# Kernel optimization log

Measured on AMD Instinct MI355X. Metric: run time of the kernel, lower is better.

The kernel has to match this reference:

```python
import jax, jax.numpy as jnp
import numpy as np

# Pitch / YIN hyperparameters (match init_kwargs)
SR = 8000
HOP = int(round(0.01 * SR))        # 80 samples per hop (hop_time=0.01)
F0_MIN = 60
F0_MAX = 400
THRESH = 0.2
TAU_MIN = SR // F0_MAX             # 20  (smallest lag / highest pitch)
TAU_MAX = SR // F0_MIN             # 133 (largest lag / lowest pitch)
W = TAU_MAX                        # YIN integration window
FRAME_LEN = 2 * TAU_MAX            # need W + TAU_MAX samples per frame


def _yin_f0(x):
    """Batched YIN pitch estimator. x: [B, n_samples] -> f0: [B, n_frames-1].

    Vectorizes the original per-sample Python loop over the whole batch and
    all frames in one pass (difference fn -> CMNDF -> thresholded lag pick).
    """
    B, n = x.shape
    n_frames = 1 + (n - FRAME_LEN) // HOP

    # Frame the signal: [B, F, FRAME_LEN]
    starts = jnp.arange(n_frames) * HOP
    idx = starts[:, None] + jnp.arange(FRAME_LEN)[None, :]
    frames = x[:, idx]

    # Difference function d(tau) = sum_j (x[j] - x[j+tau])^2, tau in [0, TAU_MAX]
    taus = jnp.arange(TAU_MAX + 1)
    sidx = taus[:, None] + jnp.arange(W)[None, :]          # [T+1, W]
    shifted = frames[:, :, sidx]                           # [B, F, T+1, W]
    base = frames[:, :, None, :W]                          # [B, F, 1,  W]
    d = jnp.sum((base - shifted) ** 2, axis=-1)            # [B, F, T+1]

    # Cumulative-mean-normalized difference function (CMNDF)
    eps = jnp.asarray(1e-8, x.dtype)
    cum = jnp.cumsum(d[..., 1:], axis=-1)
    tnum = jnp.arange(1, TAU_MAX + 1, dtype=x.dtype)
    cmndf = d[..., 1:] * tnum / jnp.maximum(cum, eps)      # tau = 1..TAU_MAX
    cmndf = jnp.concatenate([jnp.ones_like(cmndf[..., :1]), cmndf], axis=-1)

    # First lag below threshold (restricted to valid pitch range); else unvoiced
    tau_idx = jnp.arange(TAU_MAX + 1)
    cand = (cmndf < THRESH) & (tau_idx >= TAU_MIN)         # [B, F, T+1]
    voiced = jnp.any(cand, axis=-1)
    tau = jnp.argmax(cand, axis=-1)                        # first True
    f0 = jnp.where(
        voiced,
        jnp.asarray(SR, x.dtype) / jnp.maximum(tau, 1).astype(x.dtype),
        jnp.zeros((), x.dtype),
    )
    # Original forward drops the last frame per sample: f0[0, :-1]
    return f0[:, :-1]


def setup_inputs() -> dict:
    key = jax.random.key(0)
    x = jax.random.normal(key, (8, 80000), dtype=jnp.float32)
    return {"x": x}


def reference(x):
    return _yin_f0(x)
```

## Files before the change

### kernel.cpp

```cpp
#include <hip/hip_runtime.h>


#define NF_OUT 996
#define NSAMP  80000
#define BPB    249
#define TH     0.2f
#define EPS    1e-8f
#define INF_I  0x7FFFFFFF

template<int CTRL>
__device__ __forceinline__ float dpp_add16(float x) {
    int t = __builtin_amdgcn_update_dpp(0, __builtin_bit_cast(int, x), CTRL, 0xF, 0xF, false);
    return x + __builtin_bit_cast(float, t);
}
template<int CTRL>
__device__ __forceinline__ int dpp_min16(int x) {
    int t = __builtin_amdgcn_update_dpp(INF_I, x, CTRL, 0xF, 0xF, false);
    return t < x ? t : x;
}
__device__ __forceinline__ float scan16_add(float v) {
    v = dpp_add16<0x111>(v);
    v = dpp_add16<0x112>(v);
    v = dpp_add16<0x114>(v);
    v = dpp_add16<0x118>(v);
    return v;
}
__device__ __forceinline__ int red16_min(int v) {
    v = dpp_min16<0x111>(v);
    v = dpp_min16<0x112>(v);
    v = dpp_min16<0x114>(v);
    v = dpp_min16<0x118>(v);
    return v;
}

#define MAC8(FR, W0, W1, W2) do { float d_;                                    \
    d_=FR.x-W0.y; a1=fmaf(d_,d_,a1); d_=FR.x-W0.z; a2=fmaf(d_,d_,a2);          \
    d_=FR.x-W0.w; a3=fmaf(d_,d_,a3); d_=FR.x-W1.x; a4=fmaf(d_,d_,a4);          \
    d_=FR.x-W1.y; a5=fmaf(d_,d_,a5); d_=FR.x-W1.z; a6=fmaf(d_,d_,a6);          \
    d_=FR.x-W1.w; a7=fmaf(d_,d_,a7); d_=FR.x-W2.x; a8=fmaf(d_,d_,a8);          \
    d_=FR.y-W0.z; a1=fmaf(d_,d_,a1); d_=FR.y-W0.w; a2=fmaf(d_,d_,a2);          \
    d_=FR.y-W1.x; a3=fmaf(d_,d_,a3); d_=FR.y-W1.y; a4=fmaf(d_,d_,a4);          \
    d_=FR.y-W1.z; a5=fmaf(d_,d_,a5); d_=FR.y-W1.w; a6=fmaf(d_,d_,a6);          \
    d_=FR.y-W2.x; a7=fmaf(d_,d_,a7); d_=FR.y-W2.y; a8=fmaf(d_,d_,a8);          \
    d_=FR.z-W0.w; a1=fmaf(d_,d_,a1); d_=FR.z-W1.x; a2=fmaf(d_,d_,a2);          \
    d_=FR.z-W1.y; a3=fmaf(d_,d_,a3); d_=FR.z-W1.z; a4=fmaf(d_,d_,a4);          \
    d_=FR.z-W1.w; a5=fmaf(d_,d_,a5); d_=FR.z-W2.x; a6=fmaf(d_,d_,a6);          \
    d_=FR.z-W2.y; a7=fmaf(d_,d_,a7); d_=FR.z-W2.z; a8=fmaf(d_,d_,a8);          \
    d_=FR.w-W1.x; a1=fmaf(d_,d_,a1); d_=FR.w-W1.y; a2=fmaf(d_,d_,a2);          \
    d_=FR.w-W1.z; a3=fmaf(d_,d_,a3); d_=FR.w-W1.w; a4=fmaf(d_,d_,a4);          \
    d_=FR.w-W2.x; a5=fmaf(d_,d_,a5); d_=FR.w-W2.y; a6=fmaf(d_,d_,a6);          \
    d_=FR.w-W2.z; a7=fmaf(d_,d_,a7); d_=FR.w-W2.w; a8=fmaf(d_,d_,a8);          \
} while (0)

__global__ __launch_bounds__(64) void yin_kernel(const float* __restrict__ x,
                                                 float* __restrict__ out) {
    const int bx = blockIdx.x;
    const int b  = bx / BPB;
    const int fb = bx - b * BPB;
    const float* __restrict__ xrow = x + (size_t)b * NSAMP + (size_t)fb * 320;

    __shared__ __align__(16) float sch[512];
    const int t = threadIdx.x;
    *(float4*)(sch + 4 * t)       = *(const float4*)(xrow + 4 * t);
    *(float4*)(sch + 4 * t + 256) = *(const float4*)(xrow + 4 * t + 256);
    __syncthreads();

    const int q  = t >> 4;
    const int l4 = t & 15;
    const float* f  = sch + 80 * q;
    const float* gp = f + 8 * l4;

    float4 R0 = *(const float4*)(gp);
    float4 R1 = *(const float4*)(gp + 4);
    float4 R2 = *(const float4*)(gp + 8);
    float4 R3;
    const float4 S0 = R0, S1 = R1;
    float a1=0.f,a2=0.f,a3=0.f,a4=0.f,a5=0.f,a6=0.f,a7=0.f,a8=0.f;

    for (int c = 0; c < 32; c += 4) {
        float4 FR;
        R3 = *(const float4*)(gp + 4*c + 12); FR = *(const float4*)(f + 4*c);      MAC8(FR, R0, R1, R2);
        R0 = *(const float4*)(gp + 4*c + 16); FR = *(const float4*)(f + 4*c + 4);  MAC8(FR, R1, R2, R3);
        R1 = *(const float4*)(gp + 4*c + 20); FR = *(const float4*)(f + 4*c + 8);  MAC8(FR, R2, R3, R0);
        R2 = *(const float4*)(gp + 4*c + 24); FR = *(const float4*)(f + 4*c + 12); MAC8(FR, R3, R0, R1);
    }
    const float4 R35 = *(const float4*)(gp + 140);
    {
        float4 FR = *(const float4*)(f + 128);
        MAC8(FR, R0, R1, R2);
    }
    {
        float frx = f[132];
        float d_;
        d_=frx-R1.y; a1=fmaf(d_,d_,a1); d_=frx-R1.z; a2=fmaf(d_,d_,a2);
        d_=frx-R1.w; a3=fmaf(d_,d_,a3); d_=frx-R2.x; a4=fmaf(d_,d_,a4);
        d_=frx-R2.y; a5=fmaf(d_,d_,a5); d_=frx-R2.z; a6=fmaf(d_,d_,a6);
        d_=frx-R2.w; a7=fmaf(d_,d_,a7); d_=frx-R35.x; a8=fmaf(d_,d_,a8);
    }

    float SA[8]  = {S0.x,S0.y,S0.z,S0.w,S1.x,S1.y,S1.z,S1.w};
    float WA[13] = {R0.x,R0.y,R0.z,R0.w,R1.x,R1.y,R1.z,R1.w,
                    R2.x,R2.y,R2.z,R2.w,R35.x};
    float p[5] = {0.f,0.f,0.f,0.f,0.f};
    #pragma unroll
    for (int k = 0; k < 5; ++k) {
        #pragma unroll
        for (int r = 0; r < 8; ++r) {
            float d_ = SA[r] - WA[1 + k + r];
            p[k] = fmaf(d_, d_, p[k]);
        }
    }
    if (l4 < 5) {
        float fA = f[128 + l4];
        #pragma unroll
        for (int k = 0; k < 5; ++k) {
            float d_ = fA - f[257 + l4 + k];
            p[k] = fmaf(d_, d_, p[k]);
        }
    }
    #pragma unroll
    for (int k = 0; k < 5; ++k) p[k] = scan16_add(p[k]);

    float s1=a1, s2=s1+a2, s3=s2+a3, s4=s3+a4, s5=s4+a5, s6=s5+a6, s7=s6+a7, s8=s7+a8;
    float incl = scan16_add(s8);
    float excl = incl - s8;
    float c1=excl+s1, c2=excl+s2, c3=excl+s3, c4=excl+s4,
          c5=excl+s5, c6=excl+s6, c7=excl+s7, c8=excl+s8;

    int best = INF_I;
    const int tb = 8 * l4;
    if (tb+1 >= 20 && a1*(float)(tb+1) < TH*fmaxf(c1,EPS)) best = tb+1;
    if (best==INF_I && tb+2 >= 20 && a2*(float)(tb+2) < TH*fmaxf(c2,EPS)) best = tb+2;
    if (best==INF_I && tb+3 >= 20 && a3*(float)(tb+3) < TH*fmaxf(c3,EPS)) best = tb+3;
    if (best==INF_I && tb+4 >= 20 && a4*(float)(tb+4) < TH*fmaxf(c4,EPS)) best = tb+4;
    if (best==INF_I && tb+5 >= 20 && a5*(float)(tb+5) < TH*fmaxf(c5,EPS)) best = tb+5;
    if (best==INF_I && tb+6 >= 20 && a6*(float)(tb+6) < TH*fmaxf(c6,EPS)) best = tb+6;
    if (best==INF_I && tb+7 >= 20 && a7*(float)(tb+7) < TH*fmaxf(c7,EPS)) best = tb+7;
    if (best==INF_I && tb+8 >= 20 && a8*(float)(tb+8) < TH*fmaxf(c8,EPS)) best = tb+8;
    best = red16_min(best);

    if (l4 == 15) {
        float cum = c8;
        #pragma unroll
        for (int k = 0; k < 5; ++k) {
            cum += p[k];
            if (p[k] * (float)(129 + k) < TH * fmaxf(cum, EPS))
                best = (best < 129 + k) ? best : (129 + k);
        }
        out[(size_t)b * NF_OUT + fb * 4 + q] =
            (best == INF_I) ? 0.0f : 8000.0f / (float)best;
    }
}

extern "C" void kernel_launch(void* const* d_in, const int* in_sizes, int n_in,
                              void* d_out, int out_size, void* d_ws, size_t ws_size,
                              hipStream_t stream) {
    (void)in_sizes; (void)n_in; (void)d_ws; (void)ws_size; (void)out_size;
    const float* x = (const float*)d_in[0];
    float* out = (float*)d_out;
    yin_kernel<<<dim3(8 * BPB), dim3(64), 0, stream>>>(x, out);
}
```

Baseline: 16.41 us.

## Compute YIN difference via autocorrelation plus energy prefix sums

Expands (x_j - x_{j+tau})^2 into energy terms minus twice the cross-correlation, so the inner loop does one FMA per lag/sample instead of a subtract plus an FMA. The shifted-window energy for each lag comes from the frame energy plus an exclusive scan of squared-sample differences across lanes. This cuts VALU work in the hot loop but adds catastrophic-cancellation risk in float32 for the difference function near zero, which could change threshold decisions.

```diff
diff --git a/kernel.cpp b/kernel.cpp
--- a/kernel.cpp
+++ b/kernel.cpp
@@ -33,23 +33,25 @@
     return v;
 }
 
-#define MAC8(FR, W0, W1, W2) do { float d_;                                    \
-    d_=FR.x-W0.y; a1=fmaf(d_,d_,a1); d_=FR.x-W0.z; a2=fmaf(d_,d_,a2);          \
-    d_=FR.x-W0.w; a3=fmaf(d_,d_,a3); d_=FR.x-W1.x; a4=fmaf(d_,d_,a4);          \
-    d_=FR.x-W1.y; a5=fmaf(d_,d_,a5); d_=FR.x-W1.z; a6=fmaf(d_,d_,a6);          \
-    d_=FR.x-W1.w; a7=fmaf(d_,d_,a7); d_=FR.x-W2.x; a8=fmaf(d_,d_,a8);          \
-    d_=FR.y-W0.z; a1=fmaf(d_,d_,a1); d_=FR.y-W0.w; a2=fmaf(d_,d_,a2);          \
-    d_=FR.y-W1.x; a3=fmaf(d_,d_,a3); d_=FR.y-W1.y; a4=fmaf(d_,d_,a4);          \
-    d_=FR.y-W1.z; a5=fmaf(d_,d_,a5); d_=FR.y-W1.w; a6=fmaf(d_,d_,a6);          \
-    d_=FR.y-W2.x; a7=fmaf(d_,d_,a7); d_=FR.y-W2.y; a8=fmaf(d_,d_,a8);          \
-    d_=FR.z-W0.w; a1=fmaf(d_,d_,a1); d_=FR.z-W1.x; a2=fmaf(d_,d_,a2);          \
-    d_=FR.z-W1.y; a3=fmaf(d_,d_,a3); d_=FR.z-W1.z; a4=fmaf(d_,d_,a4);          \
-    d_=FR.z-W1.w; a5=fmaf(d_,d_,a5); d_=FR.z-W2.x; a6=fmaf(d_,d_,a6);          \
-    d_=FR.z-W2.y; a7=fmaf(d_,d_,a7); d_=FR.z-W2.z; a8=fmaf(d_,d_,a8);          \
-    d_=FR.w-W1.x; a1=fmaf(d_,d_,a1); d_=FR.w-W1.y; a2=fmaf(d_,d_,a2);          \
-    d_=FR.w-W1.z; a3=fmaf(d_,d_,a3); d_=FR.w-W1.w; a4=fmaf(d_,d_,a4);          \
-    d_=FR.w-W2.x; a5=fmaf(d_,d_,a5); d_=FR.w-W2.y; a6=fmaf(d_,d_,a6);          \
-    d_=FR.w-W2.z; a7=fmaf(d_,d_,a7); d_=FR.w-W2.w; a8=fmaf(d_,d_,a8);          \
+#define MACR8(FR, W0, W1, W2) do {                                             \
+    r1=fmaf(FR.x,W0.y,r1); r2=fmaf(FR.x,W0.z,r2);                              \
+    r3=fmaf(FR.x,W0.w,r3); r4=fmaf(FR.x,W1.x,r4);                              \
+    r5=fmaf(FR.x,W1.y,r5); r6=fmaf(FR.x,W1.z,r6);                              \
+    r7=fmaf(FR.x,W1.w,r7); r8=fmaf(FR.x,W2.x,r8);                              \
+    r1=fmaf(FR.y,W0.z,r1); r2=fmaf(FR.y,W0.w,r2);                              \
+    r3=fmaf(FR.y,W1.x,r3); r4=fmaf(FR.y,W1.y,r4);                              \
+    r5=fmaf(FR.y,W1.z,r5); r6=fmaf(FR.y,W1.w,r6);                              \
+    r7=fmaf(FR.y,W2.x,r7); r8=fmaf(FR.y,W2.y,r8);                              \
+    r1=fmaf(FR.z,W0.w,r1); r2=fmaf(FR.z,W1.x,r2);                              \
+    r3=fmaf(FR.z,W1.y,r3); r4=fmaf(FR.z,W1.z,r4);                              \
+    r5=fmaf(FR.z,W1.w,r5); r6=fmaf(FR.z,W2.x,r6);                              \
+    r7=fmaf(FR.z,W2.y,r7); r8=fmaf(FR.z,W2.z,r8);                              \
+    r1=fmaf(FR.w,W1.x,r1); r2=fmaf(FR.w,W1.y,r2);                              \
+    r3=fmaf(FR.w,W1.z,r3); r4=fmaf(FR.w,W1.w,r4);                              \
+    r5=fmaf(FR.w,W2.x,r5); r6=fmaf(FR.w,W2.y,r6);                              \
+    r7=fmaf(FR.w,W2.z,r7); r8=fmaf(FR.w,W2.w,r8);                              \
+    QF=fmaf(FR.x,FR.x,QF); QF=fmaf(FR.y,FR.y,QF);                              \
+    QF=fmaf(FR.z,FR.z,QF); QF=fmaf(FR.w,FR.w,QF);                              \
 } while (0)
 
 __global__ __launch_bounds__(64) void yin_kernel(const float* __restrict__ x,
@@ -75,28 +77,55 @@
     float4 R2 = *(const float4*)(gp + 8);
     float4 R3;
     const float4 S0 = R0, S1 = R1;
-    float a1=0.f,a2=0.f,a3=0.f,a4=0.f,a5=0.f,a6=0.f,a7=0.f,a8=0.f;
+    float r1=0.f,r2=0.f,r3=0.f,r4=0.f,r5=0.f,r6=0.f,r7=0.f,r8=0.f,QF=0.f;
 
     for (int c = 0; c < 32; c += 4) {
         float4 FR;
-        R3 = *(const float4*)(gp + 4*c + 12); FR = *(const float4*)(f + 4*c);      MAC8(FR, R0, R1, R2);
-        R0 = *(const float4*)(gp + 4*c + 16); FR = *(const float4*)(f + 4*c + 4);  MAC8(FR, R1, R2, R3);
-        R1 = *(const float4*)(gp + 4*c + 20); FR = *(const float4*)(f + 4*c + 8);  MAC8(FR, R2, R3, R0);
-        R2 = *(const float4*)(gp + 4*c + 24); FR = *(const float4*)(f + 4*c + 12); MAC8(FR, R3, R0, R1);
+        R3 = *(const float4*)(gp + 4*c + 12); FR = *(const float4*)(f + 4*c);      MACR8(FR, R0, R1, R2);
+        R0 = *(const float4*)(gp + 4*c + 16); FR = *(const float4*)(f + 4*c + 4);  MACR8(FR, R1, R2, R3);
+        R1 = *(const float4*)(gp + 4*c + 20); FR = *(const float4*)(f + 4*c + 8);  MACR8(FR, R2, R3, R0);
+        R2 = *(const float4*)(gp + 4*c + 24); FR = *(const float4*)(f + 4*c + 12); MACR8(FR, R3, R0, R1);
     }
     const float4 R35 = *(const float4*)(gp + 140);
     {
         float4 FR = *(const float4*)(f + 128);
-        MAC8(FR, R0, R1, R2);
+        MACR8(FR, R0, R1, R2);
     }
+    const float frx = f[132];
     {
-        float frx = f[132];
-        float d_;
-        d_=frx-R1.y; a1=fmaf(d_,d_,a1); d_=frx-R1.z; a2=fmaf(d_,d_,a2);
-        d_=frx-R1.w; a3=fmaf(d_,d_,a3); d_=frx-R2.x; a4=fmaf(d_,d_,a4);
-        d_=frx-R2.y; a5=fmaf(d_,d_,a5); d_=frx-R2.z; a6=fmaf(d_,d_,a6);
-        d_=frx-R2.w; a7=fmaf(d_,d_,a7); d_=frx-R35.x; a8=fmaf(d_,d_,a8);
+        r1=fmaf(frx,R1.y,r1); r2=fmaf(frx,R1.z,r2);
+        r3=fmaf(frx,R1.w,r3); r4=fmaf(frx,R2.x,r4);
+        r5=fmaf(frx,R2.y,r5); r6=fmaf(frx,R2.z,r6);
+        r7=fmaf(frx,R2.w,r7); r8=fmaf(frx,R35.x,r8);
+        QF = fmaf(frx, frx, QF);
     }
+    const float EA = QF;
+
+    float hi[8] = {R1.y,R1.z,R1.w,R2.x,R2.y,R2.z,R2.w,R35.x};
+    float lo[8] = {S0.x,S0.y,S0.z,S0.w,S1.x,S1.y,S1.z,S1.w};
+    float P1,P2,P3,P4,P5,P6,P7,P8;
+    {
+        float D;
+        D = fmaf(hi[0],hi[0], -(lo[0]*lo[0])); P1 = D;
+        D = fmaf(hi[1],hi[1], -(lo[1]*lo[1])); P2 = P1 + D;
+        D = fmaf(hi[2],hi[2], -(lo[2]*lo[2])); P3 = P2 + D;
+        D = fmaf(hi[3],hi[3], -(lo[3]*lo[3])); P4 = P3 + D;
+        D = fmaf(hi[4],hi[4], -(lo[4]*lo[4])); P5 = P4 + D;
+        D = fmaf(hi[5],hi[5], -(lo[5]*lo[5])); P6 = P5 + D;
+        D = fmaf(hi[6],hi[6], -(lo[6]*lo[6])); P7 = P6 + D;
+        D = fmaf(hi[7],hi[7], -(lo[7]*lo[7])); P8 = P7 + D;
+    }
+    float inclD = scan16_add(P8);
+    float exclD = inclD - P8;
+    const float base = 2.0f * EA + exclD;
+    float a1 = fmaf(-2.f, r1, base + P1);
+    float a2 = fmaf(-2.f, r2, base + P2);
+    float a3 = fmaf(-2.f, r3, base + P3);
+    float a4 = fmaf(-2.f, r4, base + P4);
+    float a5 = fmaf(-2.f, r5, base + P5);
+    float a6 = fmaf(-2.f, r6, base + P6);
+    float a7 = fmaf(-2.f, r7, base + P7);
+    float a8 = fmaf(-2.f, r8, base + P8);
 
     float SA[8]  = {S0.x,S0.y,S0.z,S0.w,S1.x,S1.y,S1.z,S1.w};
     float WA[13] = {R0.x,R0.y,R0.z,R0.w,R1.x,R1.y,R1.z,R1.w,
```

New measurement: 19.58 us. 1.19x slower.
